# Kernel optimization log

Measured on AMD Instinct MI355X. Metric: run time of the kernel, lower is better.

Reference implementation:

```python
import jax, jax.numpy as jnp
import numpy as np

T, N, C = 512, 64, 512
H, P = 1024, 512


def setup_inputs() -> dict:
    key = jax.random.key(0)
    ks = jax.random.split(key, 7)
    x = jax.random.normal(ks[0], (T, N, C), dtype=jnp.float32)
    # lengths in [1, T]
    lengths = jax.random.randint(ks[1], (N,), 1, T + 1, dtype=jnp.int64)
    s = 0.02  # small init like houyi_init
    wx_w = jax.random.normal(ks[2], (4 * H, C), dtype=jnp.float32) * s
    wx_b = jax.random.normal(ks[3], (4 * H,), dtype=jnp.float32) * s
    wr_w = jax.random.normal(ks[4], (4 * H, P), dtype=jnp.float32) * s
    wo_w = jax.random.normal(ks[5], (P, H), dtype=jnp.float32) * s
    wc = jax.random.normal(ks[6], (1, 3 * H), dtype=jnp.float32) * s
    return {"x": x, "lengths": lengths, "wx_w": wx_w, "wx_b": wx_b,
            "wr_w": wr_w, "wo_w": wo_w, "wc": wc}


def reference(x, lengths, wx_w, wx_b, wr_w, wo_w, wc):
    Tt, Nn, _ = x.shape
    Hh = wc.shape[1] // 3
    Pp = wo_w.shape[0]
    wc_i = wc[:, :Hh]
    wc_f = wc[:, Hh:2 * Hh]
    wc_o = wc[:, 2 * Hh:3 * Hh]
    # Precompute input contributions for all timesteps: (T,N,4H)
    pre = jnp.einsum('tnc,gc->tng', x, wx_w) + wx_b

    def step(carry, pre_t):
        c_prev, r_prev = carry
        g = pre_t + r_prev @ wr_w.T  # (N,4H)
        i_o, f_o, o_o, c_o = jnp.split(g, 4, axis=-1)
        in_gate = jax.nn.sigmoid(i_o + wc_i * c_prev)
        forget_gate = jax.nn.sigmoid(f_o + wc_f * c_prev)
        c_cur = forget_gate * c_prev + in_gate * jnp.tanh(c_o)
        out_gate = jax.nn.sigmoid(o_o + wc_o * c_cur)
        r_t = (out_gate * jnp.tanh(c_cur)) @ wo_w.T  # (N,P)
        return (c_cur, r_t), r_t

    c0 = jnp.zeros((Nn, Hh), dtype=x.dtype)
    r0 = jnp.zeros((Nn, Pp), dtype=x.dtype)
    _, out = jax.lax.scan(step, (c0, r0), pre)  # (T,N,P)
    # mask padded positions (t >= length) to zero
    mask = jnp.arange(Tt)[:, None] >= lengths[None, :]  # (T,N)
    return jnp.where(mask[:, :, None], jnp.zeros((), dtype=out.dtype), out)
```

## Files before the change

kernel.cpp:

```cpp
#include <hip/hip_runtime.h>
#include <hip/hip_bf16.h>
#include <cstdio>

#define TT 512
#define NN 64
#define CC 512
#define HH 1024
#define PP 512
#define GG 4096
#define MPRE (TT*NN)
#define TC 256
#define TCM (TC*NN)
#define NB 64

typedef __attribute__((ext_vector_type(8))) short short8;
typedef __attribute__((ext_vector_type(4))) float floatx4;

__device__ __forceinline__ unsigned short f2bf(float f) {
  union { float f; unsigned u; } v; v.f = f;
  unsigned r = v.u + 0x7fffu + ((v.u >> 16) & 1u);
  return (unsigned short)(r >> 16);
}
__device__ __forceinline__ float bf2f(unsigned short u) {
  union { unsigned u; float f; } v; v.u = ((unsigned)u) << 16; return v.f;
}
__device__ __forceinline__ float sigm(float x) { return 1.f / (1.f + __expf(-x)); }
__device__ __forceinline__ float tanha(float x) { return 1.f - 2.f / (__expf(2.f * x) + 1.f); }

typedef const __attribute__((address_space(1))) void gvoid_t;
typedef __attribute__((address_space(3))) void lvoid_t;
__device__ __forceinline__ void gl2lds16(const void* g, void* l) {
  __builtin_amdgcn_global_load_lds((gvoid_t*)g, (lvoid_t*)l, 16, 0, 0);
}

__global__ void cast_f32_bf16(const float* __restrict__ src, unsigned short* __restrict__ dst, int n) {
  int i = (blockIdx.x * 256 + threadIdx.x) * 4;
  if (i < n) {
    float4 v = *(const float4*)(src + i);
    ushort4 o;
    o.x = f2bf(v.x); o.y = f2bf(v.y); o.z = f2bf(v.z); o.w = f2bf(v.w);
    *(ushort4*)(dst + i) = o;
  }
}

__global__ void transpose_cast(const float* __restrict__ src, unsigned short* __restrict__ dst) {
  int idx = blockIdx.x * 256 + threadIdx.x;
  if (idx < HH * PP) {
    int h = idx >> 9, p = idx & 511;
    dst[idx] = f2bf(src[p * HH + h]);
  }
}

__global__ __launch_bounds__(256) void gemm_bt(
    const unsigned short* __restrict__ A, const unsigned short* __restrict__ B,
    const float* __restrict__ bias, unsigned short* __restrict__ C,
    int M, int N, int K, int writeT)
{
  __shared__ __align__(16) unsigned short As[128 * 32];
  __shared__ __align__(16) unsigned short Bs[128 * 32];
  const int tid = threadIdx.x;
  const int l = tid & 63, w = tid >> 6;
  const int wm = w >> 1, wn = w & 1;
  const int lane16 = l & 15, quad = l >> 4;
  const int rowA0 = blockIdx.x * 128, rowB0 = blockIdx.y * 128;
  floatx4 acc[4][4] = {};
  for (int kk = 0; kk < K; kk += 32) {
    __syncthreads();
#pragma unroll
    for (int r = 0; r < 2; ++r) {
      const int e = r * 256 + tid;
      const int row = e >> 2, kgrp = (e & 3) << 3;
      gl2lds16(A + (size_t)(rowA0 + row) * K + kk + kgrp, As + (r * 256 + w * 64) * 8);
      gl2lds16(B + (size_t)(rowB0 + row) * K + kk + kgrp, Bs + (r * 256 + w * 64) * 8);
    }
    __syncthreads();
    short8 af[4], bf[4];
#pragma unroll
    for (int mt = 0; mt < 4; ++mt) af[mt] = *(const short8*)&As[(wm * 64 + mt * 16 + lane16) * 32 + quad * 8];
#pragma unroll
    for (int nt = 0; nt < 4; ++nt) bf[nt] = *(const short8*)&Bs[(wn * 64 + nt * 16 + lane16) * 32 + quad * 8];
#pragma unroll
    for (int mt = 0; mt < 4; ++mt)
#pragma unroll
      for (int nt = 0; nt < 4; ++nt)
        acc[mt][nt] = __builtin_amdgcn_mfma_f32_16x16x32_bf16(af[mt], bf[nt], acc[mt][nt], 0, 0, 0);
  }
#pragma unroll
  for (int mt = 0; mt < 4; ++mt) {
    const int m0 = rowA0 + wm * 64 + mt * 16 + quad * 4;
#pragma unroll
    for (int nt = 0; nt < 4; ++nt) {
      const int col = rowB0 + wn * 64 + nt * 16 + lane16;
      const float bv = bias ? bias[col] : 0.f;
      if (writeT) {
        ushort4 o;
        o.x = f2bf(acc[mt][nt][0] + bv); o.y = f2bf(acc[mt][nt][1] + bv);
        o.z = f2bf(acc[mt][nt][2] + bv); o.w = f2bf(acc[mt][nt][3] + bv);
        *(ushort4*)(C + (size_t)col * M + m0) = o;
      } else {
#pragma unroll
        for (int j = 0; j < 4; ++j) C[(size_t)(m0 + j) * N + col] = f2bf(acc[mt][nt][j] + bv);
      }
    }
  }
}

__global__ __launch_bounds__(256, 1) void lstm_rec(
    const unsigned short* __restrict__ preC,
    const unsigned short* __restrict__ Wc,
    const unsigned short* __restrict__ wo,
    const float* __restrict__ wcp,
    const void* __restrict__ lengths,
    unsigned long long* __restrict__ act2,
    float* __restrict__ c_buf,
    float* __restrict__ out,
    unsigned* __restrict__ flags,
    int t0, int t1, int last)
{
  __shared__ float g4[4][64][65];
  __shared__ float r4[4][32][17];
  const int tid = threadIdx.x, b = blockIdx.x;
  const int l = tid & 63, w = tid >> 6;
  const int lane16 = l & 15, quad = l >> 4;
  const int ptile = b & 31, kgr = b >> 5;
  const int ntA = 2 * kgr, ntB = ntA + 1;

  const int* L32 = (const int*)lengths;
  const bool is64 = (L32[1] == 0);

  short8 bbr[4][8];
#pragma unroll
  for (int gt = 0; gt < 4; ++gt)
#pragma unroll
    for (int kst = 0; kst < 8; ++kst)
      bbr[gt][kst] = *(const short8*)&Wc[(size_t)(gt * 1024 + b * 16 + lane16) * 1024
                                         + w * 256 + kst * 32 + quad * 8];

  const unsigned short* worow = wo + (size_t)(ptile * 16 + lane16) * 1024 + w * 256 + quad * 8;

  const int hb = b * 16 + 4 * w;
  float cst[4], wci[4], wcf[4], wco[4];
#pragma unroll
  for (int kk = 0; kk < 4; ++kk) {
    cst[kk] = c_buf[l * HH + hb + kk];
    wci[kk] = wcp[hb + kk];
    wcf[kk] = wcp[1024 + hb + kk];
    wco[kk] = wcp[2048 + hb + kk];
  }
  const int base_t = w * 4096 + quad * 128 + lane16 * 2;
  const int pq = (2 * b + (w >> 1)) * 128 + l * 2 + (w & 1);

  const int nr = tid & 31, ph = tid >> 5;
  const int n_out = kgr * 32 + nr;
  const int ln_out = is64 ? (int)((const long long*)lengths)[n_out] : L32[n_out];

  float pvc[4][4], pvn[4][4];
  {
    const int trel = l;
#pragma unroll
    for (int g = 0; g < 4; ++g)
#pragma unroll
      for (int kk = 0; kk < 4; ++kk)
        pvc[g][kk] = bf2f(preC[(size_t)(g * 1024 + hb + kk) * TCM + trel]);
  }

#define LOADK(BUF, KST)                                                                  \
  _Pragma("unroll") for (int nt_ = 0; nt_ < 4; ++nt_) {                                  \
    Aq[BUF][nt_][0] = __hip_atomic_load(aPq + (KST) * 512 + nt_ * 32,                    \
                                        __ATOMIC_RELAXED, __HIP_MEMORY_SCOPE_AGENT);     \
    Aq[BUF][nt_][1] = __hip_atomic_load(aPq + (KST) * 512 + nt_ * 32 + 1,                \
                                        __ATOMIC_RELAXED, __HIP_MEMORY_SCOPE_AGENT);     \
  }

  for (int t = t0; t <= t1; ++t) {
    if (t == t1 && !last) break;
    const bool gate_on = (t < t1);
    const unsigned long long* aPq = act2 + (size_t)((t + 1) & 1) * 16384 + base_t;

    floatx4 accg4[4][4] = {};
    floatx4 acco4[2] = {};
    unsigned long long Aq[2][4][2];
    LOADK(0, 0)
#pragma unroll
    for (int kst = 0; kst < 8; ++kst) {
      if (kst < 7) LOADK((kst + 1) & 1, kst + 1)
      short8 wf = *(const short8*)(worow + kst * 32);
#pragma unroll
      for (int nt = 0; nt < 4; ++nt) {
        union { unsigned long long q[2]; short8 s; } u;
        u.q[0] = Aq[kst & 1][nt][0]; u.q[1] = Aq[kst & 1][nt][1];
#pragma unroll
        for (int gt = 0; gt < 4; ++gt)
          accg4[nt][gt] = __builtin_amdgcn_mfma_f32_16x16x32_bf16(u.s, bbr[gt][kst], accg4[nt][gt], 0, 0, 0);
        if (nt == ntA) acco4[0] = __builtin_amdgcn_mfma_f32_16x16x32_bf16(u.s, wf, acco4[0], 0, 0, 0);
        if (nt == ntB) acco4[1] = __builtin_amdgcn_mfma_f32_16x16x32_bf16(u.s, wf, acco4[1], 0, 0, 0);
      }
    }

    if (gate_on) {
#pragma unroll
      for (int nt = 0; nt < 4; ++nt)
#pragma unroll
        for (int gt = 0; gt < 4; ++gt)
#pragma unroll
          for (int j = 0; j < 4; ++j)
            g4[w][nt * 16 + quad * 4 + j][gt * 16 + lane16] = accg4[nt][gt][j];
      __syncthreads();

      float hh[4];
      unsigned long long packed = 0;
#pragma unroll
      for (int kk = 0; kk < 4; ++kk) {
        const int c0 = 0 * 16 + 4 * w + kk, c1 = 1 * 16 + 4 * w + kk;
        const int c2 = 2 * 16 + 4 * w + kk, c3 = 3 * 16 + 4 * w + kk;
        float gi = g4[0][l][c0] + g4[1][l][c0] + g4[2][l][c0] + g4[3][l][c0] + pvc[0][kk];
        float gf = g4[0][l][c1] + g4[1][l][c1] + g4[2][l][c1] + g4[3][l][c1] + pvc[1][kk];
        float go = g4[0][l][c2] + g4[1][l][c2] + g4[2][l][c2] + g4[3][l][c2] + pvc[2][kk];
        float gc = g4[0][l][c3] + g4[1][l][c3] + g4[2][l][c3] + g4[3][l][c3] + pvc[3][kk];
        float ig = sigm(gi + wci[kk] * cst[kk]);
        float fg = sigm(gf + wcf[kk] * cst[kk]);
        float cc = fg * cst[kk] + ig * tanha(gc);
        float og = sigm(go + wco[kk] * cc);
        cst[kk] = cc;
        hh[kk] = og * tanha(cc);
        packed |= (unsigned long long)f2bf(hh[kk]) << (16 * kk);
      }
      __hip_atomic_store(act2 + (size_t)(t & 1) * 16384 + pq, packed,
                         __ATOMIC_RELAXED, __HIP_MEMORY_SCOPE_AGENT);

      __builtin_amdgcn_s_waitcnt(0);
      __syncthreads();
      if (tid == 0) {
        __atomic_signal_fence(__ATOMIC_SEQ_CST);
        __hip_atomic_store(&flags[b], (unsigned)(t + 1),
                           __ATOMIC_RELAXED, __HIP_MEMORY_SCOPE_AGENT);
      }
      if (t + 1 < t1) {
        const int trel = (t + 1 - t0) * NN + l;
#pragma unroll
        for (int g = 0; g < 4; ++g)
#pragma unroll
          for (int kk = 0; kk < 4; ++kk)
            pvn[g][kk] = bf2f(preC[(size_t)(g * 1024 + hb + kk) * TCM + trel]);
      }
    }

#pragma unroll
    for (int i = 0; i < 2; ++i)
#pragma unroll
      for (int j = 0; j < 4; ++j)
        r4[w][i * 16 + quad * 4 + j][lane16] = acco4[i][j];
    __syncthreads();
    if (t > 0) {
      const int pl0 = ph * 2;
      float o0 = r4[0][nr][pl0]     + r4[1][nr][pl0]     + r4[2][nr][pl0]     + r4[3][nr][pl0];
      float o1 = r4[0][nr][pl0 + 1] + r4[1][nr][pl0 + 1] + r4[2][nr][pl0 + 1] + r4[3][nr][pl0 + 1];
      if ((t - 1) >= ln_out) { o0 = 0.f; o1 = 0.f; }
      *(float2*)&out[(size_t)((t - 1) * NN + n_out) * PP + ptile * 16 + pl0] = make_float2(o0, o1);
    }

    if (gate_on) {
      if (w == 0) {
        const unsigned tgt = (unsigned)(t + 1);
        while (1) {
          unsigned f = __hip_atomic_load(&flags[l], __ATOMIC_RELAXED, __HIP_MEMORY_SCOPE_AGENT);
          if (__all(f >= tgt)) break;
          __builtin_amdgcn_s_sleep(1);
        }
        __atomic_signal_fence(__ATOMIC_SEQ_CST);
      }
      __syncthreads();
      if (t + 1 < t1) {
#pragma unroll
        for (int g = 0; g < 4; ++g)
#pragma unroll
          for (int kk = 0; kk < 4; ++kk)
            pvc[g][kk] = pvn[g][kk];
      }
    }
  }
#pragma unroll
  for (int kk = 0; kk < 4; ++kk) c_buf[l * HH + hb + kk] = cst[kk];
#undef LOADK
}

extern "C" void kernel_launch(void* const* d_in, const int* in_sizes, int n_in,
                              void* d_out, int out_size, void* d_ws, size_t ws_size,
                              hipStream_t stream) {
  (void)in_sizes; (void)n_in; (void)out_size;
  const float* x    = (const float*)d_in[0];
  const void*  len  = d_in[1];
  const float* wx_w = (const float*)d_in[2];
  const float* wx_b = (const float*)d_in[3];
  const float* wr_w = (const float*)d_in[4];
  const float* wo_w = (const float*)d_in[5];
  const float* wc   = (const float*)d_in[6];
  float* out = (float*)d_out;

  char* ws = (char*)d_ws; size_t off = 0;
  auto alloc = [&](size_t b) { void* p = ws + off; off += (b + 255) & ~(size_t)255; return p; };
  unsigned short* x_bf  = (unsigned short*)alloc((size_t)MPRE * CC * 2);
  unsigned short* wx_bf = (unsigned short*)alloc((size_t)GG * CC * 2);
  unsigned short* wr_bf = (unsigned short*)alloc((size_t)GG * PP * 2);
  unsigned short* wo_bf = (unsigned short*)alloc((size_t)PP * HH * 2);
  unsigned short* woT   = (unsigned short*)alloc((size_t)HH * PP * 2);
  unsigned short* Wc_bf = (unsigned short*)alloc((size_t)GG * HH * 2);
  unsigned short* preC  = (unsigned short*)alloc((size_t)GG * TCM * 2);
  unsigned long long* act2 = (unsigned long long*)alloc((size_t)2 * 16384 * 8);
  float*          c_buf = (float*)alloc((size_t)NN * HH * 4);
  unsigned* flags = (unsigned*)alloc(512);
  if (off > ws_size) {
    fprintf(stderr, "kernel_launch: workspace too small (%zu needed, %zu given)\n", off, ws_size);
    return;
  }

  hipMemsetAsync(act2, 0, (size_t)2 * 16384 * 8 + (size_t)NN * HH * 4 + 512, stream);

  int n1 = MPRE * CC; cast_f32_bf16<<<dim3((n1 / 4 + 255) / 256), dim3(256), 0, stream>>>(x, x_bf, n1);
  int n2 = GG * CC;   cast_f32_bf16<<<dim3((n2 / 4 + 255) / 256), dim3(256), 0, stream>>>(wx_w, wx_bf, n2);
  int n3 = GG * PP;   cast_f32_bf16<<<dim3((n3 / 4 + 255) / 256), dim3(256), 0, stream>>>(wr_w, wr_bf, n3);
  int n4 = PP * HH;   cast_f32_bf16<<<dim3((n4 / 4 + 255) / 256), dim3(256), 0, stream>>>(wo_w, wo_bf, n4);
  transpose_cast<<<dim3((HH * PP + 255) / 256), dim3(256), 0, stream>>>(wo_w, woT);

  gemm_bt<<<dim3(GG / 128, HH / 128), dim3(256), 0, stream>>>(wr_bf, woT, nullptr, Wc_bf, GG, HH, PP, 0);

  for (int chunk = 0; chunk < TT / TC; ++chunk) {
    const int t0 = chunk * TC, t1 = t0 + TC;
    const int last = (t1 == TT) ? 1 : 0;
    gemm_bt<<<dim3(TCM / 128, GG / 128), dim3(256), 0, stream>>>(
        x_bf + (size_t)t0 * NN * CC, wx_bf, wx_b, preC, TCM, GG, CC, 1);

    lstm_rec<<<dim3(NB), dim3(256), 0, stream>>>(
        preC, Wc_bf, wo_bf, wc, len, act2, c_buf, out, flags, t0, t1, last);
  }
}
```

Baseline: 3.334 ms.

## Defer output reduction off the critical path and pad inter-block flags

Moves the reduction and store of the projected output for step t-1 to after the next step's activation loads have been issued, so it overlaps the recurrent matmul instead of sitting between the gate computation and the grid barrier. All waves now spin on the flags rather than only wave 0, which removes one __syncthreads per step. The per-block flags are padded to separate cache lines to reduce contention. Epilogue handling is added for chunk boundaries, which adds complexity and some risk of getting the output ordering wrong.

```diff
diff --git a/kernel.cpp b/kernel.cpp
--- a/kernel.cpp
+++ b/kernel.cpp
@@ -12,6 +12,7 @@
 #define TC 256
 #define TCM (TC*NN)
 #define NB 64
+#define FSTR 32
 
 typedef __attribute__((ext_vector_type(8))) short short8;
 typedef __attribute__((ext_vector_type(4))) float floatx4;
@@ -153,6 +154,7 @@
   const int nr = tid & 31, ph = tid >> 5;
   const int n_out = kgr * 32 + nr;
   const int ln_out = is64 ? (int)((const long long*)lengths)[n_out] : L32[n_out];
+  const int pl0 = ph * 2;
 
   float pvc[4][4], pvn[4][4];
   {
@@ -172,8 +174,19 @@
                                         __ATOMIC_RELAXED, __HIP_MEMORY_SCOPE_AGENT);     \
   }
 
+#define OUTSTORE(ROW)                                                                    \
+  {                                                                                      \
+    float o0 = r4[0][nr][pl0]     + r4[1][nr][pl0]     + r4[2][nr][pl0]     + r4[3][nr][pl0];     \
+    float o1 = r4[0][nr][pl0 + 1] + r4[1][nr][pl0 + 1] + r4[2][nr][pl0 + 1] + r4[3][nr][pl0 + 1]; \
+    if ((ROW) >= ln_out) { o0 = 0.f; o1 = 0.f; }                                         \
+    *(float2*)&out[(size_t)((ROW) * NN + n_out) * PP + ptile * 16 + pl0] = make_float2(o0, o1);   \
+  }
+
   for (int t = t0; t <= t1; ++t) {
-    if (t == t1 && !last) break;
+    if (t == t1 && !last) {
+      OUTSTORE(t - 2)
+      break;
+    }
     const bool gate_on = (t < t1);
     const unsigned long long* aPq = act2 + (size_t)((t + 1) & 1) * 16384 + base_t;
 
@@ -181,6 +194,10 @@
     floatx4 acco4[2] = {};
     unsigned long long Aq[2][4][2];
     LOADK(0, 0)
+
+    if (t > t0 && t >= 2) OUTSTORE(t - 2)
+    __syncthreads();
+
 #pragma unroll
     for (int kst = 0; kst < 8; ++kst) {
       if (kst < 7) LOADK((kst + 1) & 1, kst + 1)
@@ -196,6 +213,12 @@
         if (nt == ntB) acco4[1] = __builtin_amdgcn_mfma_f32_16x16x32_bf16(u.s, wf, acco4[1], 0, 0, 0);
       }
     }
+
+#pragma unroll
+    for (int i = 0; i < 2; ++i)
+#pragma unroll
+      for (int j = 0; j < 4; ++j)
+        r4[w][i * 16 + quad * 4 + j][lane16] = acco4[i][j];
 
     if (gate_on) {
 #pragma unroll
@@ -232,7 +255,7 @@
       __syncthreads();
       if (tid == 0) {
         __atomic_signal_fence(__ATOMIC_SEQ_CST);
-        __hip_atomic_store(&flags[b], (unsigned)(t + 1),
+        __hip_atomic_store(&flags[b * FSTR], (unsigned)(t + 1),
                            __ATOMIC_RELAXED, __HIP_MEMORY_SCOPE_AGENT);
       }
       if (t + 1 < t1) {
@@ -243,33 +266,16 @@
           for (int kk = 0; kk < 4; ++kk)
             pvn[g][kk] = bf2f(preC[(size_t)(g * 1024 + hb + kk) * TCM + trel]);
       }
-    }
-
-#pragma unroll
-    for (int i = 0; i < 2; ++i)
-#pragma unroll
-      for (int j = 0; j < 4; ++j)
-        r4[w][i * 16 + quad * 4 + j][lane16] = acco4[i][j];
-    __syncthreads();
-    if (t > 0) {
-      const int pl0 = ph * 2;
-      float o0 = r4[0][nr][pl0]     + r4[1][nr][pl0]     + r4[2][nr][pl0]     + r4[3][nr][pl0];
-      float o1 = r4[0][nr][pl0 + 1] + r4[1][nr][pl0 + 1] + r4[2][nr][pl0 + 1] + r4[3][nr][pl0 + 1];
-      if ((t - 1) >= ln_out) { o0 = 0.f; o1 = 0.f; }
-      *(float2*)&out[(size_t)((t - 1) * NN + n_out) * PP + ptile * 16 + pl0] = make_float2(o0, o1);
-    }
-
-    if (gate_on) {
-      if (w == 0) {
+
+      {
         const unsigned tgt = (unsigned)(t + 1);
         while (1) {
-          unsigned f = __hip_atomic_load(&flags[l], __ATOMIC_RELAXED, __HIP_MEMORY_SCOPE_AGENT);
+          unsigned f = __hip_atomic_load(&flags[l * FSTR], __ATOMIC_RELAXED, __HIP_MEMORY_SCOPE_AGENT);
           if (__all(f >= tgt)) break;
           __builtin_amdgcn_s_sleep(1);
         }
         __atomic_signal_fence(__ATOMIC_SEQ_CST);
       }
-      __syncthreads();
       if (t + 1 < t1) {
 #pragma unroll
         for (int g = 0; g < 4; ++g)
@@ -279,9 +285,15 @@
       }
     }
   }
+
+  if (last) {
+    __syncthreads();
+    OUTSTORE(t1 - 1)
+  }
 #pragma unroll
   for (int kk = 0; kk < 4; ++kk) c_buf[l * HH + hb + kk] = cst[kk];
 #undef LOADK
+#undef OUTSTORE
 }
 
 extern "C" void kernel_launch(void* const* d_in, const int* in_sizes, int n_in,
@@ -308,13 +320,13 @@
   unsigned short* preC  = (unsigned short*)alloc((size_t)GG * TCM * 2);
   unsigned long long* act2 = (unsigned long long*)alloc((size_t)2 * 16384 * 8);
   float*          c_buf = (float*)alloc((size_t)NN * HH * 4);
-  unsigned* flags = (unsigned*)alloc(512);
+  unsigned* flags = (unsigned*)alloc((size_t)NB * FSTR * 4);
   if (off > ws_size) {
     fprintf(stderr, "kernel_launch: workspace too small (%zu needed, %zu given)\n", off, ws_size);
     return;
   }
 
-  hipMemsetAsync(act2, 0, (size_t)2 * 16384 * 8 + (size_t)NN * HH * 4 + 512, stream);
+  hipMemsetAsync(act2, 0, (size_t)2 * 16384 * 8 + (size_t)NN * HH * 4 + (size_t)NB * FSTR * 4, stream);
 
   int n1 = MPRE * CC; cast_f32_bf16<<<dim3((n1 / 4 + 255) / 256), dim3(256), 0, stream>>>(x, x_bf, n1);
   int n2 = GG * CC;   cast_f32_bf16<<<dim3((n2 / 4 + 255) / 256), dim3(256), 0, stream>>>(wx_w, wx_bf, n2);
```

New measurement: 4.133 ms. 24.0% more time.
